# Performance work log

Hardware: AMD Instinct MI355X
Metric: run time of the kernel (lower is better)

Reference implementation:

```python
import jax, jax.numpy as jnp
import numpy as np

N, D, H, E, K = 8192, 2048, 2048, 8, 2
CAP = 4096  # per-expert capacity; avg load is N*K/E = 2048, so 4096 is >40 sigma safe for uniform routing


def setup_inputs() -> dict:
    key = jax.random.key(0)
    ks = jax.random.split(key, 6)
    x = jax.random.normal(ks[0], (N, D), dtype=jnp.float32)
    expert_weights = jax.random.uniform(ks[1], (N, K), dtype=jnp.float32)
    w1 = 0.02 * jax.random.normal(ks[2], (E, D, H), dtype=jnp.float32)
    w2 = 0.02 * jax.random.normal(ks[3], (E, H, D), dtype=jnp.float32)
    w3 = 0.02 * jax.random.normal(ks[4], (E, D, H), dtype=jnp.float32)
    expert_indices = jax.random.randint(ks[5], (N, K), 0, E, dtype=jnp.int32)
    batch_size_per_expert = jnp.bincount(expert_indices.reshape(-1), length=E).astype(jnp.int32)
    return {
        "x": x,
        "expert_weights": expert_weights,
        "w1": w1,
        "w2": w2,
        "w3": w3,
        "expert_indices": expert_indices,
        "batch_size_per_expert": batch_size_per_expert,
    }


def reference(x, expert_weights, w1, w2, w3, expert_indices, batch_size_per_expert):
    n, d = x.shape
    e = w1.shape[0]
    top_k = expert_indices.shape[-1]
    nt = n * top_k

    ei = expert_indices.reshape(-1).astype(jnp.int32)   # (NT,)
    ew = expert_weights.reshape(-1)                     # (NT,)

    # indices_and_bins: stable sort of expert ids + cumsum bins
    indices = jnp.argsort(ei)            # token-copy order grouped by expert (stable)
    bin_ids = ei[indices]                # (NT,) sorted expert ids
    bins = jnp.cumsum(batch_size_per_expert)
    starts = bins - batch_size_per_expert
    pos = jnp.arange(nt, dtype=jnp.int32) - starts[bin_ids]  # slot within expert bin

    # permute: gather tokens (indices // top_k maps copy -> source token)
    tok = indices // top_k
    x_perm = x[tok]                                     # (NT, D)

    # dispatch into (E, CAP, D) buffer
    buf = jnp.zeros((e, CAP, d), x.dtype).at[bin_ids, pos].set(x_perm)

    # per-expert SwiGLU MLP: (silu(x w1) * (x w3)) w2
    g = jax.nn.silu(jnp.einsum("ecd,edh->ech", buf, w1))
    u = jnp.einsum("ecd,edh->ech", buf, w3)
    out = jnp.einsum("ech,ehd->ecd", g * u, w2)         # (E, CAP, D)

    # unpermute + weighted combine (scatter-add over top_k copies)
    y_perm = out[bin_ids, pos]                          # (NT, D)
    w_perm = ew[indices]
    y = jnp.zeros_like(x).at[tok].add(y_perm * w_perm[:, None])
    return y
```

## Files before the change

kernel.cpp:

```cpp
#include <hip/hip_runtime.h>
#include <hip/hip_bf16.h>
#include <cstdio>
#include <cstdint>

#define N_TOK 8192
#define D_DIM 2048
#define H_DIM 2048
#define N_EXP 8
#define TOP_K 2
#define NT_CP (N_TOK * TOP_K)
#define BM 128
#define BN 128
#define BK 64
#define MT_MAX 32

typedef __attribute__((ext_vector_type(4))) float f32x4;
typedef __attribute__((ext_vector_type(8))) short s16x8;
typedef __attribute__((ext_vector_type(4))) short s16x4;

static constexpr size_t OFF_CNT  = 0;
static constexpr size_t OFF_ROWS = 256;
static constexpr size_t OFF_WTS  = OFF_ROWS + (size_t)(NT_CP + 128) * 4;
static constexpr size_t OFF_XB   = OFF_WTS  + (size_t)(NT_CP + 128) * 4;
static constexpr size_t OFF_ACT  = OFF_XB   + (size_t)N_TOK * D_DIM * 2;
static constexpr size_t OFF_W13T = OFF_ACT  + (size_t)(NT_CP + 128) * H_DIM * 2;
static constexpr size_t OFF_W2T  = OFF_W13T + (size_t)N_EXP * 4096 * (size_t)D_DIM * 2;
static constexpr size_t WS_NEED  = OFF_W2T  + (size_t)N_EXP * (size_t)H_DIM * D_DIM * 2;

__device__ __forceinline__ short f2bf(float f) {
    uint32_t u = __builtin_bit_cast(uint32_t, f);
    uint32_t r = (u + 0x7FFFu + ((u >> 16) & 1u)) >> 16;
    return (short)r;
}

#define GLOAD_LDS16(g, l)                                                                  \
    __builtin_amdgcn_global_load_lds((const __attribute__((address_space(1))) void*)(g),   \
                                     (__attribute__((address_space(3))) void*)(l), 16, 0, 0)

__global__ void routing_kernel(const int* __restrict__ eidx, const float* __restrict__ ew,
                               const int* __restrict__ bspe, int* __restrict__ cnt,
                               int* __restrict__ rows, float* __restrict__ wts) {
    int i = blockIdx.x * blockDim.x + threadIdx.x;
    if (i >= NT_CP) return;
    int e = eidx[i];
    int off = 0;
#pragma unroll
    for (int j = 0; j < N_EXP; ++j) off += (j < e) ? bspe[j] : 0;
    int slot = atomicAdd(&cnt[e], 1);
    rows[off + slot] = i / TOP_K;
    wts[off + slot]  = ew[i];
}

__global__ void cast_x_kernel(const float* __restrict__ x, short* __restrict__ xb) {
    int i = blockIdx.x * blockDim.x + threadIdx.x;
    const int total = N_TOK * D_DIM / 4;
    if (i >= total) return;
    f32x4 v = ((const f32x4*)x)[i];
    s16x4 o;
    o.x = f2bf(v.x); o.y = f2bf(v.y); o.z = f2bf(v.z); o.w = f2bf(v.w);
    ((s16x4*)xb)[i] = o;
}

__global__ void transpose_cast_fused(const float* __restrict__ w1, const float* __restrict__ w3,
                                     const float* __restrict__ w2, short* __restrict__ w13t,
                                     short* __restrict__ w2t) {
    __shared__ float t[64][65];
    const int slab = blockIdx.z;
    const int mat = slab >> 3, e = slab & 7;
    const float* in = (mat == 0 ? w1 : (mat == 1 ? w3 : w2)) + (size_t)e * D_DIM * H_DIM;
    short* out = (mat == 2) ? (w2t + (size_t)e * D_DIM * H_DIM)
                            : (w13t + (size_t)e * 4096 * D_DIM);
    const int r0 = blockIdx.y * 64, c0 = blockIdx.x * 64;
    const int tid = threadIdx.x;

#pragma unroll
    for (int p = 0; p < 4; ++p) {
        int r = p * 16 + (tid >> 4);
        int c4 = (tid & 15) * 4;
        f32x4 v = *(const f32x4*)&in[(size_t)(r0 + r) * 2048 + c0 + c4];
        t[r][c4 + 0] = v.x; t[r][c4 + 1] = v.y; t[r][c4 + 2] = v.z; t[r][c4 + 3] = v.w;
    }
    __syncthreads();
#pragma unroll
    for (int p = 0; p < 2; ++p) {
        int c = c0 + p * 32 + (tid >> 3);
        int r8 = (tid & 7) * 8;
        s16x8 o;
#pragma unroll
        for (int j = 0; j < 8; ++j) o[j] = f2bf(t[r8 + j][c - c0]);
        int row2 = (mat == 2) ? c : (((c >> 4) << 5) + ((mat == 1) ? 16 : 0) + (c & 15));
        *(s16x8*)&out[(size_t)row2 * 2048 + r0 + r8] = o;
    }
}

__launch_bounds__(256, 2)
__global__ void gemm1_kernel(const short* __restrict__ xb, const short* __restrict__ w13t,
                             const int* __restrict__ rows, const int* __restrict__ bspe,
                             short* __restrict__ act) {
    const int e = blockIdx.z;
    const int cnt_e = bspe[e];
    const int mt = blockIdx.y;
    if (mt * BM >= cnt_e) return;
    int off_e = 0;
#pragma unroll
    for (int j = 0; j < N_EXP; ++j) off_e += (j < e) ? bspe[j] : 0;
    const int p0 = off_e + mt * BM;
    const int bn0 = blockIdx.x * BN;
    int valid_rows = cnt_e - mt * BM;
    if (valid_rows > BM) valid_rows = BM;

    __shared__ short sA[BM * BK];
    __shared__ short sB[BN * BK];

    const int tid = threadIdx.x;
    const int lane = tid & 63;
    const int wid = tid >> 6;

    const short* a_src[4];
#pragma unroll
    for (int i = 0; i < 4; ++i) {
        int r = i * 32 + (tid >> 3);
        int tok = (r < valid_rows) ? rows[p0 + r] : rows[p0];
        a_src[i] = xb + (size_t)tok * D_DIM + (tid & 7) * 8;
    }
    const short* b_src = w13t + ((size_t)e * 4096 + bn0 + (tid >> 3)) * D_DIM + (tid & 7) * 8;

    f32x4 acc[4][4];
#pragma unroll
    for (int mi = 0; mi < 4; ++mi)
#pragma unroll
        for (int ni = 0; ni < 4; ++ni) acc[mi][ni] = (f32x4){0.f, 0.f, 0.f, 0.f};

    const int wm = (wid >> 1) * 64;
    const int wn = (wid & 1) * 64;

    for (int k0 = 0; k0 < D_DIM; k0 += BK) {
#pragma unroll
        for (int i = 0; i < 4; ++i)
            GLOAD_LDS16(a_src[i] + k0, &sA[(i * 32 + wid * 8) * BK]);
#pragma unroll
        for (int i = 0; i < 4; ++i)
            GLOAD_LDS16(b_src + (size_t)i * 32 * D_DIM + k0, &sB[(i * 32 + wid * 8) * BK]);
        __syncthreads();
#pragma unroll
        for (int kk = 0; kk < 2; ++kk) {
            s16x8 af[4], bf[4];
#pragma unroll
            for (int mi = 0; mi < 4; ++mi)
                af[mi] = *(const s16x8*)&sA[(wm + mi * 16 + (lane & 15)) * BK + kk * 32 + (lane >> 4) * 8];
#pragma unroll
            for (int ni = 0; ni < 4; ++ni)
                bf[ni] = *(const s16x8*)&sB[(wn + ni * 16 + (lane & 15)) * BK + kk * 32 + (lane >> 4) * 8];
#pragma unroll
            for (int mi = 0; mi < 4; ++mi)
#pragma unroll
                for (int ni = 0; ni < 4; ++ni)
                    acc[mi][ni] = __builtin_amdgcn_mfma_f32_16x16x32_bf16(af[mi], bf[ni], acc[mi][ni], 0, 0, 0);
        }
        __syncthreads();
    }

    const int hbase = (bn0 + wn) >> 1;
#pragma unroll
    for (int mi = 0; mi < 4; ++mi) {
#pragma unroll
        for (int j = 0; j < 4; ++j) {
            int row = wm + mi * 16 + (lane >> 4) * 4 + j;
            if (row < valid_rows) {
                size_t base = (size_t)(p0 + row) * H_DIM + hbase + (lane & 15);
#pragma unroll
                for (int p = 0; p < 2; ++p) {
                    float g = acc[mi][2 * p][j];
                    float u = acc[mi][2 * p + 1][j];
                    float s = g / (1.0f + __expf(-g));
                    act[base + p * 16] = f2bf(s * u);
                }
            }
        }
    }
}

__launch_bounds__(256, 2)
__global__ void gemm2_kernel(const short* __restrict__ act, const short* __restrict__ w2t,
                             const int* __restrict__ rows, const float* __restrict__ wts,
                             const int* __restrict__ bspe, float* __restrict__ y) {
    const int e = blockIdx.z;
    const int cnt_e = bspe[e];
    const int mt = blockIdx.y;
    if (mt * BM >= cnt_e) return;
    int off_e = 0;
#pragma unroll
    for (int j = 0; j < N_EXP; ++j) off_e += (j < e) ? bspe[j] : 0;
    const int p0 = off_e + mt * BM;
    const int bn0 = blockIdx.x * BN;
    int valid_rows = cnt_e - mt * BM;
    if (valid_rows > BM) valid_rows = BM;

    __shared__ short sA[BM * BK];
    __shared__ short sB[BN * BK];

    const int tid = threadIdx.x;
    const int lane = tid & 63;
    const int wid = tid >> 6;

    const short* a_src = act + (size_t)(p0 + (tid >> 3)) * H_DIM + (tid & 7) * 8;
    const short* b_src = w2t + ((size_t)e * D_DIM + bn0 + (tid >> 3)) * H_DIM + (tid & 7) * 8;

    f32x4 acc[4][4];
#pragma unroll
    for (int mi = 0; mi < 4; ++mi)
#pragma unroll
        for (int ni = 0; ni < 4; ++ni) acc[mi][ni] = (f32x4){0.f, 0.f, 0.f, 0.f};

    const int wm = (wid >> 1) * 64;
    const int wn = (wid & 1) * 64;

    for (int k0 = 0; k0 < H_DIM; k0 += BK) {
#pragma unroll
        for (int i = 0; i < 4; ++i)
            GLOAD_LDS16(a_src + (size_t)i * 32 * H_DIM + k0, &sA[(i * 32 + wid * 8) * BK]);
#pragma unroll
        for (int i = 0; i < 4; ++i)
            GLOAD_LDS16(b_src + (size_t)i * 32 * H_DIM + k0, &sB[(i * 32 + wid * 8) * BK]);
        __syncthreads();
#pragma unroll
        for (int kk = 0; kk < 2; ++kk) {
            s16x8 af[4], bf[4];
#pragma unroll
            for (int mi = 0; mi < 4; ++mi)
                af[mi] = *(const s16x8*)&sA[(wm + mi * 16 + (lane & 15)) * BK + kk * 32 + (lane >> 4) * 8];
#pragma unroll
            for (int ni = 0; ni < 4; ++ni)
                bf[ni] = *(const s16x8*)&sB[(wn + ni * 16 + (lane & 15)) * BK + kk * 32 + (lane >> 4) * 8];
#pragma unroll
            for (int mi = 0; mi < 4; ++mi)
#pragma unroll
                for (int ni = 0; ni < 4; ++ni)
                    acc[mi][ni] = __builtin_amdgcn_mfma_f32_16x16x32_bf16(af[mi], bf[ni], acc[mi][ni], 0, 0, 0);
        }
        __syncthreads();
    }

#pragma unroll
    for (int mi = 0; mi < 4; ++mi) {
#pragma unroll
        for (int j = 0; j < 4; ++j) {
            int row = wm + mi * 16 + (lane >> 4) * 4 + j;
            if (row < valid_rows) {
                int p = p0 + row;
                int tok = rows[p];
                float w = wts[p];
                float* ybase = y + (size_t)tok * D_DIM + bn0 + wn + (lane & 15);
#pragma unroll
                for (int ni = 0; ni < 4; ++ni)
                    atomicAdd(ybase + ni * 16, acc[mi][ni][j] * w);
            }
        }
    }
}

extern "C" void kernel_launch(void* const* d_in, const int* in_sizes, int n_in,
                              void* d_out, int out_size, void* d_ws, size_t ws_size,
                              hipStream_t stream) {
    const float* x    = (const float*)d_in[0];
    const float* ew   = (const float*)d_in[1];
    const float* w1   = (const float*)d_in[2];
    const float* w2   = (const float*)d_in[3];
    const float* w3   = (const float*)d_in[4];
    const int* eidx   = (const int*)d_in[5];
    const int* bspe   = (const int*)d_in[6];
    float* y          = (float*)d_out;
    char* ws          = (char*)d_ws;

    if (ws_size < WS_NEED) {
        fprintf(stderr, "[kernel] ws too small: have %zu need %zu\n", ws_size, WS_NEED);
        return;
    }

    int*   cnt  = (int*)(ws + OFF_CNT);
    int*   rows = (int*)(ws + OFF_ROWS);
    float* wts  = (float*)(ws + OFF_WTS);
    short* xb   = (short*)(ws + OFF_XB);
    short* act  = (short*)(ws + OFF_ACT);
    short* w13t = (short*)(ws + OFF_W13T);
    short* w2t  = (short*)(ws + OFF_W2T);

    hipMemsetAsync(cnt, 0, 256, stream);
    hipMemsetAsync(y, 0, (size_t)N_TOK * D_DIM * 4, stream);

    routing_kernel<<<NT_CP / 256, 256, 0, stream>>>(eidx, ew, bspe, cnt, rows, wts);
    cast_x_kernel<<<(N_TOK * D_DIM / 4) / 256, 256, 0, stream>>>(x, xb);

    transpose_cast_fused<<<dim3(2048 / 64, 2048 / 64, 24), 256, 0, stream>>>(w1, w3, w2, w13t, w2t);

    gemm1_kernel<<<dim3(4096 / BN, MT_MAX, N_EXP), 256, 0, stream>>>(xb, w13t, rows, bspe, act);
    gemm2_kernel<<<dim3(D_DIM / BN, MT_MAX, N_EXP), 256, 0, stream>>>(act, w2t, rows, wts, bspe, y);
}
```

Measured before the change: 1.072 ms.

## Merge expert GEMMs into 256x256 double-buffered swizzled 8-wave kernel template

Replaces the two 128x128 single-buffered GEMM kernels with one templated kernel using 256x256 tiles, 512 threads (8 waves), and a two-stage LDS double buffer with vmcnt-based waiting so global loads overlap MFMA work. LDS rows are XOR-swizzled to avoid bank conflicts, and MFMA phases are bracketed with s_setprio. The larger tiles raise arithmetic intensity per weight load but use 128KB of LDS and many accumulators, which limits occupancy, and partially filled expert tiles waste more work.

```diff
diff --git a/kernel.cpp b/kernel.cpp
--- a/kernel.cpp
+++ b/kernel.cpp
@@ -9,10 +9,6 @@
 #define N_EXP 8
 #define TOP_K 2
 #define NT_CP (N_TOK * TOP_K)
-#define BM 128
-#define BN 128
-#define BK 64
-#define MT_MAX 32
 
 typedef __attribute__((ext_vector_type(4))) float f32x4;
 typedef __attribute__((ext_vector_type(8))) short s16x8;
@@ -93,170 +89,166 @@
     }
 }
 
-__launch_bounds__(256, 2)
-__global__ void gemm1_kernel(const short* __restrict__ xb, const short* __restrict__ w13t,
-                             const int* __restrict__ rows, const int* __restrict__ bspe,
-                             short* __restrict__ act) {
+template <int MODE>
+__launch_bounds__(512, 2)
+__global__ void gemm_8p(const short* __restrict__ Aglob, const short* __restrict__ Bglob,
+                        const int* __restrict__ rows, const float* __restrict__ wts,
+                        const int* __restrict__ bspe, short* __restrict__ act_out,
+                        float* __restrict__ y) {
     const int e = blockIdx.z;
     const int cnt_e = bspe[e];
     const int mt = blockIdx.y;
-    if (mt * BM >= cnt_e) return;
+    if (mt * 256 >= cnt_e) return;
     int off_e = 0;
 #pragma unroll
     for (int j = 0; j < N_EXP; ++j) off_e += (j < e) ? bspe[j] : 0;
-    const int p0 = off_e + mt * BM;
-    const int bn0 = blockIdx.x * BN;
-    int valid_rows = cnt_e - mt * BM;
-    if (valid_rows > BM) valid_rows = BM;
-
-    __shared__ short sA[BM * BK];
-    __shared__ short sB[BN * BK];
+    const int p0 = off_e + mt * 256;
+    const int bn0 = blockIdx.x * 256;
+    int valid_rows = cnt_e - mt * 256;
+    if (valid_rows > 256) valid_rows = 256;
+
+    __shared__ short smem[65536];
 
     const int tid = threadIdx.x;
     const int lane = tid & 63;
     const int wid = tid >> 6;
-
+    const int wm = (wid >> 2) * 128;
+    const int wn = (wid & 3) * 64;
+
+    const int srow = tid >> 3;
+    const int sblk = (tid & 7) ^ (srow & 7);
+    const int NROWS_B = (MODE == 0) ? 4096 : 2048;
     const short* a_src[4];
+    const short* b_src[4];
 #pragma unroll
     for (int i = 0; i < 4; ++i) {
-        int r = i * 32 + (tid >> 3);
-        int tok = (r < valid_rows) ? rows[p0 + r] : rows[p0];
-        a_src[i] = xb + (size_t)tok * D_DIM + (tid & 7) * 8;
-    }
-    const short* b_src = w13t + ((size_t)e * 4096 + bn0 + (tid >> 3)) * D_DIM + (tid & 7) * 8;
-
-    f32x4 acc[4][4];
-#pragma unroll
-    for (int mi = 0; mi < 4; ++mi)
+        int r = i * 64 + srow;
+        if (MODE == 0) {
+            int tok = (r < valid_rows) ? rows[p0 + r] : rows[p0];
+            a_src[i] = Aglob + (size_t)tok * 2048 + sblk * 8;
+        } else {
+            int rp = (r < valid_rows) ? (p0 + r) : p0;
+            a_src[i] = Aglob + (size_t)rp * 2048 + sblk * 8;
+        }
+        b_src[i] = Bglob + ((size_t)e * NROWS_B + bn0 + r) * 2048 + sblk * 8;
+    }
+
+#define STAGE(buf, k0)                                                        \
+    do {                                                                      \
+        short* da_ = smem + (buf) * 32768;                                    \
+        short* db_ = da_ + 16384;                                             \
+        _Pragma("unroll")                                                     \
+        for (int i_ = 0; i_ < 4; ++i_) {                                      \
+            GLOAD_LDS16(a_src[i_] + (k0), &da_[(i_ * 512 + tid) * 8]);        \
+            GLOAD_LDS16(b_src[i_] + (k0), &db_[(i_ * 512 + tid) * 8]);        \
+        }                                                                     \
+    } while (0)
+
+    f32x4 acc[8][4];
+#pragma unroll
+    for (int mi = 0; mi < 8; ++mi)
 #pragma unroll
         for (int ni = 0; ni < 4; ++ni) acc[mi][ni] = (f32x4){0.f, 0.f, 0.f, 0.f};
 
-    const int wm = (wid >> 1) * 64;
-    const int wn = (wid & 1) * 64;
-
-    for (int k0 = 0; k0 < D_DIM; k0 += BK) {
-#pragma unroll
-        for (int i = 0; i < 4; ++i)
-            GLOAD_LDS16(a_src[i] + k0, &sA[(i * 32 + wid * 8) * BK]);
-#pragma unroll
-        for (int i = 0; i < 4; ++i)
-            GLOAD_LDS16(b_src + (size_t)i * 32 * D_DIM + k0, &sB[(i * 32 + wid * 8) * BK]);
-        __syncthreads();
-#pragma unroll
-        for (int kk = 0; kk < 2; ++kk) {
-            s16x8 af[4], bf[4];
-#pragma unroll
-            for (int mi = 0; mi < 4; ++mi)
-                af[mi] = *(const s16x8*)&sA[(wm + mi * 16 + (lane & 15)) * BK + kk * 32 + (lane >> 4) * 8];
-#pragma unroll
-            for (int ni = 0; ni < 4; ++ni)
-                bf[ni] = *(const s16x8*)&sB[(wn + ni * 16 + (lane & 15)) * BK + kk * 32 + (lane >> 4) * 8];
-#pragma unroll
-            for (int mi = 0; mi < 4; ++mi)
-#pragma unroll
-                for (int ni = 0; ni < 4; ++ni)
-                    acc[mi][ni] = __builtin_amdgcn_mfma_f32_16x16x32_bf16(af[mi], bf[ni], acc[mi][ni], 0, 0, 0);
-        }
-        __syncthreads();
-    }
-
-    const int hbase = (bn0 + wn) >> 1;
-#pragma unroll
-    for (int mi = 0; mi < 4; ++mi) {
-#pragma unroll
-        for (int j = 0; j < 4; ++j) {
-            int row = wm + mi * 16 + (lane >> 4) * 4 + j;
-            if (row < valid_rows) {
-                size_t base = (size_t)(p0 + row) * H_DIM + hbase + (lane & 15);
-#pragma unroll
-                for (int p = 0; p < 2; ++p) {
-                    float g = acc[mi][2 * p][j];
-                    float u = acc[mi][2 * p + 1][j];
-                    float s = g / (1.0f + __expf(-g));
-                    act[base + p * 16] = f2bf(s * u);
+#define PHASE(bufbase, mh, nh)                                                             \
+    do {                                                                                   \
+        const char* pa_ = (const char*)(bufbase);                                          \
+        const char* pb_ = pa_ + 32768;                                                     \
+        s16x8 af_[4][2], bf_[2][2];                                                        \
+        _Pragma("unroll")                                                                  \
+        for (int mi_ = 0; mi_ < 4; ++mi_) {                                                \
+            int row_ = wm + (mh) * 64 + mi_ * 16 + (lane & 15);                            \
+            _Pragma("unroll")                                                              \
+            for (int kk_ = 0; kk_ < 2; ++kk_) {                                            \
+                int colb_ = ((kk_ * 4 + (lane >> 4)) ^ (row_ & 7)) * 16;                   \
+                af_[mi_][kk_] = *(const s16x8*)(pa_ + row_ * 128 + colb_);                 \
+            }                                                                              \
+        }                                                                                  \
+        _Pragma("unroll")                                                                  \
+        for (int nj_ = 0; nj_ < 2; ++nj_) {                                                \
+            int row_ = wn + (nh) * 32 + nj_ * 16 + (lane & 15);                            \
+            _Pragma("unroll")                                                              \
+            for (int kk_ = 0; kk_ < 2; ++kk_) {                                            \
+                int colb_ = ((kk_ * 4 + (lane >> 4)) ^ (row_ & 7)) * 16;                   \
+                bf_[nj_][kk_] = *(const s16x8*)(pb_ + row_ * 128 + colb_);                 \
+            }                                                                              \
+        }                                                                                  \
+        __builtin_amdgcn_s_setprio(1);                                                     \
+        _Pragma("unroll")                                                                  \
+        for (int kk_ = 0; kk_ < 2; ++kk_)                                                  \
+            _Pragma("unroll")                                                              \
+            for (int mi_ = 0; mi_ < 4; ++mi_)                                              \
+                _Pragma("unroll")                                                          \
+                for (int nj_ = 0; nj_ < 2; ++nj_)                                          \
+                    acc[(mh) * 4 + mi_][(nh) * 2 + nj_] = __builtin_amdgcn_mfma_f32_16x16x32_bf16( \
+                        af_[mi_][kk_], bf_[nj_][kk_], acc[(mh) * 4 + mi_][(nh) * 2 + nj_], 0, 0, 0); \
+        __builtin_amdgcn_s_setprio(0);                                                     \
+    } while (0)
+
+    STAGE(0, 0);
+    STAGE(1, 64);
+
+    for (int t = 0; t < 31; ++t) {
+        asm volatile("s_waitcnt vmcnt(8)" ::: "memory");
+        __builtin_amdgcn_s_barrier();
+        const short* bb = smem + (t & 1) * 32768;
+        PHASE(bb, 0, 0);
+        PHASE(bb, 0, 1);
+        PHASE(bb, 1, 0);
+        PHASE(bb, 1, 1);
+        asm volatile("" ::: "memory");
+        __builtin_amdgcn_s_barrier();
+        if (t + 2 < 32) STAGE(t & 1, (t + 2) * 64);
+    }
+    asm volatile("s_waitcnt vmcnt(0)" ::: "memory");
+    __builtin_amdgcn_s_barrier();
+    {
+        const short* bb = smem + 32768;
+        PHASE(bb, 0, 0);
+        PHASE(bb, 0, 1);
+        PHASE(bb, 1, 0);
+        PHASE(bb, 1, 1);
+    }
+
+    if (MODE == 0) {
+        const int hbase = (bn0 + wn) >> 1;
+#pragma unroll
+        for (int mi = 0; mi < 8; ++mi) {
+#pragma unroll
+            for (int j = 0; j < 4; ++j) {
+                int row = wm + mi * 16 + (lane >> 4) * 4 + j;
+                if (row < valid_rows) {
+                    size_t base = (size_t)(p0 + row) * H_DIM + hbase + (lane & 15);
+#pragma unroll
+                    for (int p = 0; p < 2; ++p) {
+                        float g = acc[mi][2 * p][j];
+                        float u = acc[mi][2 * p + 1][j];
+                        float s = g / (1.0f + __expf(-g));
+                        act_out[base + p * 16] = f2bf(s * u);
+                    }
                 }
             }
         }
-    }
-}
-
-__launch_bounds__(256, 2)
-__global__ void gemm2_kernel(const short* __restrict__ act, const short* __restrict__ w2t,
-                             const int* __restrict__ rows, const float* __restrict__ wts,
-                             const int* __restrict__ bspe, float* __restrict__ y) {
-    const int e = blockIdx.z;
-    const int cnt_e = bspe[e];
-    const int mt = blockIdx.y;
-    if (mt * BM >= cnt_e) return;
-    int off_e = 0;
-#pragma unroll
-    for (int j = 0; j < N_EXP; ++j) off_e += (j < e) ? bspe[j] : 0;
-    const int p0 = off_e + mt * BM;
-    const int bn0 = blockIdx.x * BN;
-    int valid_rows = cnt_e - mt * BM;
-    if (valid_rows > BM) valid_rows = BM;
-
-    __shared__ short sA[BM * BK];
-    __shared__ short sB[BN * BK];
-
-    const int tid = threadIdx.x;
-    const int lane = tid & 63;
-    const int wid = tid >> 6;
-
-    const short* a_src = act + (size_t)(p0 + (tid >> 3)) * H_DIM + (tid & 7) * 8;
-    const short* b_src = w2t + ((size_t)e * D_DIM + bn0 + (tid >> 3)) * H_DIM + (tid & 7) * 8;
-
-    f32x4 acc[4][4];
-#pragma unroll
-    for (int mi = 0; mi < 4; ++mi)
-#pragma unroll
-        for (int ni = 0; ni < 4; ++ni) acc[mi][ni] = (f32x4){0.f, 0.f, 0.f, 0.f};
-
-    const int wm = (wid >> 1) * 64;
-    const int wn = (wid & 1) * 64;
-
-    for (int k0 = 0; k0 < H_DIM; k0 += BK) {
-#pragma unroll
-        for (int i = 0; i < 4; ++i)
-            GLOAD_LDS16(a_src + (size_t)i * 32 * H_DIM + k0, &sA[(i * 32 + wid * 8) * BK]);
-#pragma unroll
-        for (int i = 0; i < 4; ++i)
-            GLOAD_LDS16(b_src + (size_t)i * 32 * H_DIM + k0, &sB[(i * 32 + wid * 8) * BK]);
-        __syncthreads();
-#pragma unroll
-        for (int kk = 0; kk < 2; ++kk) {
-            s16x8 af[4], bf[4];
-#pragma unroll
-            for (int mi = 0; mi < 4; ++mi)
-                af[mi] = *(const s16x8*)&sA[(wm + mi * 16 + (lane & 15)) * BK + kk * 32 + (lane >> 4) * 8];
-#pragma unroll
-            for (int ni = 0; ni < 4; ++ni)
-                bf[ni] = *(const s16x8*)&sB[(wn + ni * 16 + (lane & 15)) * BK + kk * 32 + (lane >> 4) * 8];
-#pragma unroll
-            for (int mi = 0; mi < 4; ++mi)
-#pragma unroll
-                for (int ni = 0; ni < 4; ++ni)
-                    acc[mi][ni] = __builtin_amdgcn_mfma_f32_16x16x32_bf16(af[mi], bf[ni], acc[mi][ni], 0, 0, 0);
-        }
-        __syncthreads();
-    }
-
-#pragma unroll
-    for (int mi = 0; mi < 4; ++mi) {
-#pragma unroll
-        for (int j = 0; j < 4; ++j) {
-            int row = wm + mi * 16 + (lane >> 4) * 4 + j;
-            if (row < valid_rows) {
-                int p = p0 + row;
-                int tok = rows[p];
-                float w = wts[p];
-                float* ybase = y + (size_t)tok * D_DIM + bn0 + wn + (lane & 15);
-#pragma unroll
-                for (int ni = 0; ni < 4; ++ni)
-                    atomicAdd(ybase + ni * 16, acc[mi][ni][j] * w);
+    } else {
+#pragma unroll
+        for (int mi = 0; mi < 8; ++mi) {
+#pragma unroll
+            for (int j = 0; j < 4; ++j) {
+                int row = wm + mi * 16 + (lane >> 4) * 4 + j;
+                if (row < valid_rows) {
+                    int p = p0 + row;
+                    int tok = rows[p];
+                    float w = wts[p];
+                    float* yb = y + (size_t)tok * D_DIM + bn0 + wn + (lane & 15);
+#pragma unroll
+                    for (int ni = 0; ni < 4; ++ni)
+                        atomicAdd(yb + ni * 16, acc[mi][ni][j] * w);
+                }
             }
         }
     }
+#undef STAGE
+#undef PHASE
 }
 
 extern "C" void kernel_launch(void* const* d_in, const int* in_sizes, int n_in,
@@ -293,6 +285,6 @@
 
     transpose_cast_fused<<<dim3(2048 / 64, 2048 / 64, 24), 256, 0, stream>>>(w1, w3, w2, w13t, w2t);
 
-    gemm1_kernel<<<dim3(4096 / BN, MT_MAX, N_EXP), 256, 0, stream>>>(xb, w13t, rows, bspe, act);
-    gemm2_kernel<<<dim3(D_DIM / BN, MT_MAX, N_EXP), 256, 0, stream>>>(act, w2t, rows, wts, bspe, y);
-}
+    gemm_8p<0><<<dim3(4096 / 256, 16, N_EXP), 512, 0, stream>>>(xb, w13t, rows, nullptr, bspe, act, nullptr);
+    gemm_8p<1><<<dim3(2048 / 256, 16, N_EXP), 512, 0, stream>>>(act, w2t, rows, wts, bspe, nullptr, y);
+}
```

New measurement: 1.122 ms. 1.05x slower.
